# Optimization experiments

Measured on AMD Instinct MI355X. Metric: run time of the kernel, lower is better.

Reference implementation:

```python
import jax, jax.numpy as jnp
import numpy as np

B, S, H, F, E, TOPK = 2, 2048, 1024, 4096, 8, 2


def setup_inputs() -> dict:
    key = jax.random.key(0)
    k0, k1, k2, k3, k4 = jax.random.split(key, 5)
    scale = 0.02
    return {
        "hidden_states": jax.random.normal(k0, (B, S, H), dtype=jnp.float32),
        "gate_w": jax.random.normal(k1, (E, H), dtype=jnp.float32) * scale,
        "w1": jax.random.normal(k2, (E, F, H), dtype=jnp.float32) * scale,
        "w2": jax.random.normal(k3, (E, H, F), dtype=jnp.float32) * scale,
        "w3": jax.random.normal(k4, (E, F, H), dtype=jnp.float32) * scale,
        "top_k": TOPK,
    }


def reference(hidden_states, gate_w, w1, w2, w3, top_k):
    b, s, h = hidden_states.shape
    num_experts = gate_w.shape[0]
    x = hidden_states.reshape(-1, h)                      # [T,H]
    router_logits = x @ gate_w.T                          # [T,E]
    routing = jax.nn.softmax(router_logits.astype(jnp.float32), axis=-1)
    top_w, top_e = jax.lax.top_k(routing, top_k)          # [T,K]
    top_w = top_w / top_w.sum(axis=-1, keepdims=True)     # renormalize over top-k
    top_w = top_w.astype(x.dtype)
    # combine weights [T,E]: zero for unselected experts (faithful to masked dispatch)
    cw = (jax.nn.one_hot(top_e, num_experts, dtype=x.dtype) * top_w[..., None]).sum(axis=1)
    out = jnp.zeros_like(x)
    for e in range(num_experts):  # fixed, small expert count
        inter = jax.nn.silu(x @ w1[e].T) * (x @ w3[e].T)  # [T,F]
        out = out + cw[:, e:e + 1] * (inter @ w2[e].T)
    return out.reshape(b, s, h), router_logits
```

## Files before the change

### kernel.cpp

```cpp
#include <hip/hip_runtime.h>
#include <stdint.h>

#define T 4096
#define HDIM 1024
#define FDIM 4096
#define NE 8
#define MAXROWS 9216

typedef __bf16 bf16x8 __attribute__((ext_vector_type(8)));
typedef float f32x4 __attribute__((ext_vector_type(4)));

__device__ __forceinline__ unsigned short f2bf(float f) {
    unsigned u = __builtin_bit_cast(unsigned, f);
    u += 0x7FFFu + ((u >> 16) & 1u);
    return (unsigned short)(u >> 16);
}

__device__ __forceinline__ void cp16(const void* g, const void* lds) {
    __builtin_amdgcn_global_load_lds(
        (const __attribute__((address_space(1))) unsigned int*)g,
        (__attribute__((address_space(3))) unsigned int*)(unsigned int)(unsigned long long)lds,
        16, 0, 0);
}

__global__ void conv_x_k(const float* __restrict__ x, unsigned short* __restrict__ xb) {
    size_t i = ((size_t)blockIdx.x * 256 + threadIdx.x) * 8;
    float4 a = *(const float4*)(x + i);
    float4 b = *(const float4*)(x + i + 4);
    uint4 v;
    v.x = (unsigned)f2bf(a.x) | ((unsigned)f2bf(a.y) << 16);
    v.y = (unsigned)f2bf(a.z) | ((unsigned)f2bf(a.w) << 16);
    v.z = (unsigned)f2bf(b.x) | ((unsigned)f2bf(b.y) << 16);
    v.w = (unsigned)f2bf(b.z) | ((unsigned)f2bf(b.w) << 16);
    *(uint4*)(xb + i) = v;
}

__global__ void conv_w13_k(const float* __restrict__ src, unsigned short* __restrict__ dst,
                           int f0, int Fc) {
    int e = blockIdx.y;
    size_t rem = ((size_t)blockIdx.x * 256 + threadIdx.x) * 8;
    const float* s = src + ((size_t)e * FDIM + f0) * HDIM + rem;
    unsigned short* d = dst + (size_t)e * Fc * HDIM + rem;
    float4 a = *(const float4*)(s);
    float4 b = *(const float4*)(s + 4);
    uint4 v;
    v.x = (unsigned)f2bf(a.x) | ((unsigned)f2bf(a.y) << 16);
    v.y = (unsigned)f2bf(a.z) | ((unsigned)f2bf(a.w) << 16);
    v.z = (unsigned)f2bf(b.x) | ((unsigned)f2bf(b.y) << 16);
    v.w = (unsigned)f2bf(b.z) | ((unsigned)f2bf(b.w) << 16);
    *(uint4*)(d) = v;
}

__global__ void conv_w2_k(const float* __restrict__ src, unsigned short* __restrict__ dst,
                          int f0, int Fc, int fcShift) {
    int e = blockIdx.y;
    size_t idx = ((size_t)blockIdx.x * 256 + threadIdx.x) * 8;
    int h = (int)(idx >> fcShift);
    int c = (int)(idx & (size_t)(Fc - 1));
    const float* s = src + ((size_t)e * HDIM + h) * FDIM + f0 + c;
    unsigned short* d = dst + (size_t)e * HDIM * Fc + idx;
    float4 a = *(const float4*)(s);
    float4 b = *(const float4*)(s + 4);
    uint4 v;
    v.x = (unsigned)f2bf(a.x) | ((unsigned)f2bf(a.y) << 16);
    v.y = (unsigned)f2bf(a.z) | ((unsigned)f2bf(a.w) << 16);
    v.z = (unsigned)f2bf(b.x) | ((unsigned)f2bf(b.y) << 16);
    v.w = (unsigned)f2bf(b.z) | ((unsigned)f2bf(b.w) << 16);
    *(uint4*)(d) = v;
}

__global__ void router_k(const float* __restrict__ x, const float* __restrict__ gw,
                         float* __restrict__ logits_out, int* __restrict__ cnt,
                         int* __restrict__ list, float* __restrict__ wlist) {
    int w = threadIdx.x >> 6, lane = threadIdx.x & 63;
    int t = blockIdx.x * 4 + w;
    float acc[NE];
#pragma unroll
    for (int e = 0; e < NE; ++e) acc[e] = 0.f;
    for (int i = 0; i < HDIM / 64; ++i) {
        int h = i * 64 + lane;
        float xv = x[(size_t)t * HDIM + h];
#pragma unroll
        for (int e = 0; e < NE; ++e) acc[e] += xv * gw[e * HDIM + h];
    }
#pragma unroll
    for (int e = 0; e < NE; ++e)
#pragma unroll
        for (int off = 32; off; off >>= 1) acc[e] += __shfl_xor(acc[e], off);
    if (lane == 0) {
#pragma unroll
        for (int e = 0; e < NE; ++e) logits_out[(size_t)t * NE + e] = acc[e];
        int e1 = 0;
#pragma unroll
        for (int e = 1; e < NE; ++e) if (acc[e] > acc[e1]) e1 = e;
        int e2 = (e1 == 0) ? 1 : 0;
#pragma unroll
        for (int e = 0; e < NE; ++e) { if (e == e1) continue; if (acc[e] > acc[e2]) e2 = e; }
        float wa = 1.f / (1.f + expf(acc[e2] - acc[e1]));
        float wb = 1.f - wa;
        int p1 = atomicAdd(&cnt[e1], 1); list[e1 * T + p1] = t; wlist[e1 * T + p1] = wa;
        int p2 = atomicAdd(&cnt[e2], 1); list[e2 * T + p2] = t; wlist[e2 * T + p2] = wb;
    }
}

__global__ void offsets_k(const int* __restrict__ cnt, int* __restrict__ poff) {
    if (threadIdx.x == 0) {
        int o = 0; poff[0] = 0;
        for (int e = 0; e < NE; ++e) { o += ((cnt[e] + 127) >> 7) << 7; poff[e + 1] = o; }
    }
}

__global__ void compact_k(const int* __restrict__ cnt, const int* __restrict__ poff,
                          const int* __restrict__ list, const float* __restrict__ wlist,
                          int* __restrict__ tok_row, float* __restrict__ w_row) {
    int gid = blockIdx.x * 256 + threadIdx.x;
    int e = gid >> 12, i = gid & (T - 1);
    int pc = poff[e + 1] - poff[e];
    if (i < pc) {
        int row = poff[e] + i;
        if (i < cnt[e]) { tok_row[row] = list[e * T + i]; w_row[row] = wlist[e * T + i]; }
        else           { tok_row[row] = T;               w_row[row] = 0.f; }
    }
}

__global__ __launch_bounds__(256, 3) void gemm1_k(
    const unsigned short* __restrict__ xb, const unsigned short* __restrict__ wb1,
    const unsigned short* __restrict__ wb3, const int* __restrict__ tok_row,
    const int* __restrict__ poff, unsigned short* __restrict__ inter, int Fc) {

    __shared__ __align__(16) unsigned short As[128 * 64];
    __shared__ __align__(16) unsigned short B1[128 * 64];
    __shared__ __align__(16) unsigned short B3[128 * 64];
    __shared__ int toks[128];
    __shared__ int e_sh;

    int row0 = blockIdx.x * 128;
    if (row0 >= poff[NE]) return;
    int tid = threadIdx.x;
    if (tid == 0) { int e = 0; while (row0 >= poff[e + 1]) ++e; e_sh = e; }
    if (tid < 128) toks[tid] = tok_row[row0 + tid];
    __syncthreads();
    int e = e_sh;
    int fr0 = blockIdx.y * 128;
    const unsigned short* w1p = wb1 + ((size_t)e * Fc + fr0) * HDIM;
    const unsigned short* w3p = wb3 + ((size_t)e * Fc + fr0) * HDIM;

    int wv = tid >> 6, lane = tid & 63;
    int quad = lane >> 4, l16 = lane & 15;
    int wm = (wv >> 1) * 64, wn = (wv & 1) * 64;

    int sr = lane >> 3;
    int sc = (lane & 7) ^ sr;
    unsigned a_off[4];
#pragma unroll
    for (int jj = 0; jj < 4; ++jj)
        a_off[jj] = (unsigned)toks[wv * 32 + jj * 8 + sr] * HDIM + sc * 8;
    const unsigned short* w1b = w1p + (size_t)(wv * 32 + sr) * HDIM + sc * 8;
    const unsigned short* w3b = w3p + (size_t)(wv * 32 + sr) * HDIM + sc * 8;

    f32x4 acc1[4][4], acc3[4][4];
#pragma unroll
    for (int a = 0; a < 4; ++a)
#pragma unroll
        for (int b = 0; b < 4; ++b) {
            acc1[a][b] = f32x4{0.f, 0.f, 0.f, 0.f};
            acc3[a][b] = f32x4{0.f, 0.f, 0.f, 0.f};
        }

    for (int k0 = 0; k0 < HDIM; k0 += 64) {
#pragma unroll
        for (int jj = 0; jj < 4; ++jj) {
            int j = wv * 4 + jj;
            cp16(xb + a_off[jj] + k0, As + j * 512);
            cp16(w1b + (size_t)jj * 8 * HDIM + k0, B1 + j * 512);
            cp16(w3b + (size_t)jj * 8 * HDIM + k0, B3 + j * 512);
        }
        __syncthreads();
#pragma unroll
        for (int ks = 0; ks < 2; ++ks) {
            int cb0 = ks * 4 + quad;
            bf16x8 af[4];
#pragma unroll
            for (int mi = 0; mi < 4; ++mi) {
                int m = wm + mi * 16 + l16;
                af[mi] = *(const bf16x8*)(As + m * 64 + ((cb0 ^ (m & 7)) * 8));
            }
#pragma unroll
            for (int ni = 0; ni < 4; ++ni) {
                int n = wn + ni * 16 + l16;
                int boff = n * 64 + ((cb0 ^ (n & 7)) * 8);
                bf16x8 b1f = *(const bf16x8*)(B1 + boff);
                bf16x8 b3f = *(const bf16x8*)(B3 + boff);
#pragma unroll
                for (int mi = 0; mi < 4; ++mi) {
                    acc1[mi][ni] = __builtin_amdgcn_mfma_f32_16x16x32_bf16(af[mi], b1f, acc1[mi][ni], 0, 0, 0);
                    acc3[mi][ni] = __builtin_amdgcn_mfma_f32_16x16x32_bf16(af[mi], b3f, acc3[mi][ni], 0, 0, 0);
                }
            }
        }
        __syncthreads();
    }
#pragma unroll
    for (int mi = 0; mi < 4; ++mi)
#pragma unroll
        for (int ni = 0; ni < 4; ++ni)
#pragma unroll
            for (int r = 0; r < 4; ++r) {
                int m = wm + mi * 16 + quad * 4 + r;
                int n = wn + ni * 16 + l16;
                float v1 = acc1[mi][ni][r], v3 = acc3[mi][ni][r];
                float hval = (v1 / (1.f + __expf(-v1))) * v3;
                inter[(size_t)(row0 + m) * Fc + fr0 + n] = f2bf(hval);
            }
}

__global__ __launch_bounds__(256, 3) void gemm2_k(
    const unsigned short* __restrict__ inter, const unsigned short* __restrict__ wb2,
    const int* __restrict__ tok_row, const float* __restrict__ w_row,
    const int* __restrict__ poff, float* __restrict__ out, int Fc) {

    __shared__ __align__(16) unsigned short As[128 * 64];
    __shared__ __align__(16) unsigned short Bs[128 * 64];
    __shared__ int e_sh;

    int row0 = blockIdx.x * 128;
    if (row0 >= poff[NE]) return;
    int tid = threadIdx.x;
    if (tid == 0) { int e = 0; while (row0 >= poff[e + 1]) ++e; e_sh = e; }
    __syncthreads();
    int e = e_sh;
    int n0 = blockIdx.y * 128;

    int wv = tid >> 6, lane = tid & 63;
    int quad = lane >> 4, l16 = lane & 15;
    int wm = (wv >> 1) * 64, wn = (wv & 1) * 64;

    int sr = lane >> 3;
    int sc = (lane & 7) ^ sr;
    const unsigned short* a_b = inter + (size_t)(row0 + wv * 32 + sr) * Fc + sc * 8;
    const unsigned short* b_b = wb2 + ((size_t)e * HDIM + n0 + wv * 32 + sr) * Fc + sc * 8;

    f32x4 acc[4][4];
#pragma unroll
    for (int a = 0; a < 4; ++a)
#pragma unroll
        for (int b = 0; b < 4; ++b) acc[a][b] = f32x4{0.f, 0.f, 0.f, 0.f};

    for (int k0 = 0; k0 < Fc; k0 += 64) {
#pragma unroll
        for (int jj = 0; jj < 4; ++jj) {
            int j = wv * 4 + jj;
            cp16(a_b + (size_t)jj * 8 * Fc + k0, As + j * 512);
            cp16(b_b + (size_t)jj * 8 * Fc + k0, Bs + j * 512);
        }
        __syncthreads();
#pragma unroll
        for (int ks = 0; ks < 2; ++ks) {
            int cb0 = ks * 4 + quad;
            bf16x8 af[4];
#pragma unroll
            for (int mi = 0; mi < 4; ++mi) {
                int m = wm + mi * 16 + l16;
                af[mi] = *(const bf16x8*)(As + m * 64 + ((cb0 ^ (m & 7)) * 8));
            }
#pragma unroll
            for (int ni = 0; ni < 4; ++ni) {
                int n = wn + ni * 16 + l16;
                bf16x8 bf = *(const bf16x8*)(Bs + n * 64 + ((cb0 ^ (n & 7)) * 8));
#pragma unroll
                for (int mi = 0; mi < 4; ++mi)
                    acc[mi][ni] = __builtin_amdgcn_mfma_f32_16x16x32_bf16(af[mi], bf, acc[mi][ni], 0, 0, 0);
            }
        }
        __syncthreads();
    }
#pragma unroll
    for (int mi = 0; mi < 4; ++mi)
#pragma unroll
        for (int ni = 0; ni < 4; ++ni)
#pragma unroll
            for (int r = 0; r < 4; ++r) {
                int m = wm + mi * 16 + quad * 4 + r;
                int n = wn + ni * 16 + l16;
                int grow = row0 + m;
                float wr = w_row[grow];
                if (wr != 0.f) {
                    int t = tok_row[grow];
                    atomicAdd(out + (size_t)t * HDIM + n0 + n, wr * acc[mi][ni][r]);
                }
            }
}

extern "C" void kernel_launch(void* const* d_in, const int* in_sizes, int n_in,
                              void* d_out, int out_size, void* d_ws, size_t ws_size,
                              hipStream_t stream) {
    const float* x  = (const float*)d_in[0];
    const float* gw = (const float*)d_in[1];
    const float* w1 = (const float*)d_in[2];
    const float* w2 = (const float*)d_in[3];
    const float* w3 = (const float*)d_in[4];
    float* out = (float*)d_out;
    float* logits = out + (size_t)T * HDIM;

    char* ws = (char*)d_ws;
    size_t off = 0;
    auto alloc = [&](size_t b) {
        off = (off + 255) & ~(size_t)255;
        void* p = ws + off;
        off += b;
        return p;
    };
    int* cnt        = (int*)alloc(NE * 4);
    int* poff       = (int*)alloc((NE + 1) * 4);
    int* list       = (int*)alloc((size_t)NE * T * 4);
    float* wlist    = (float*)alloc((size_t)NE * T * 4);
    int* tok_row    = (int*)alloc(MAXROWS * 4);
    float* w_row    = (float*)alloc(MAXROWS * 4);
    unsigned short* xb = (unsigned short*)alloc((size_t)(T + 1) * HDIM * 2);
    size_t fixed_off = off;

    int Fc = 4096, fcShift = 12;
    for (;;) {
        size_t need = fixed_off + 3 * ((size_t)NE * Fc * HDIM * 2) + (size_t)MAXROWS * Fc * 2 + 1024;
        if (need <= ws_size || Fc == 512) break;
        Fc >>= 1; fcShift -= 1;
    }
    unsigned short* wb1 = (unsigned short*)alloc((size_t)NE * Fc * HDIM * 2);
    unsigned short* wb3 = (unsigned short*)alloc((size_t)NE * Fc * HDIM * 2);
    unsigned short* wb2 = (unsigned short*)alloc((size_t)NE * HDIM * Fc * 2);
    unsigned short* inter = (unsigned short*)alloc((size_t)MAXROWS * Fc * 2);

    hipMemsetAsync(cnt, 0, NE * 4, stream);
    hipMemsetAsync(out, 0, (size_t)T * HDIM * 4, stream);
    hipMemsetAsync(xb + (size_t)T * HDIM, 0, HDIM * 2, stream);
    conv_x_k<<<(T * HDIM / 8) / 256, 256, 0, stream>>>(x, xb);
    router_k<<<T / 4, 256, 0, stream>>>(x, gw, logits, cnt, list, wlist);
    offsets_k<<<1, 64, 0, stream>>>(cnt, poff);
    compact_k<<<NE * T / 256, 256, 0, stream>>>(cnt, poff, list, wlist, tok_row, w_row);

    int nMT = MAXROWS / 128;
    for (int f0 = 0; f0 < FDIM; f0 += Fc) {
        conv_w13_k<<<dim3(Fc / 2, NE), 256, 0, stream>>>(w1, wb1, f0, Fc);
        conv_w13_k<<<dim3(Fc / 2, NE), 256, 0, stream>>>(w3, wb3, f0, Fc);
        conv_w2_k<<<dim3(HDIM * Fc / 2048, NE), 256, 0, stream>>>(w2, wb2, f0, Fc, fcShift);
        gemm1_k<<<dim3(nMT, Fc / 128), 256, 0, stream>>>(xb, wb1, wb3, tok_row, poff, inter, Fc);
        gemm2_k<<<dim3(nMT, HDIM / 128), 256, 0, stream>>>(inter, wb2, tok_row, w_row, poff, out, Fc);
    }
}
```

Before: 847.0 us.

## Widen gemm2 tile to 128x256 with 512 threads and fuse weight conversion

gemm2 now uses 512-thread blocks computing a 128x256 output tile, so each A tile of the intermediate activations is reused across twice as many output columns, halving A reloads. The atomic epilogue is reordered so the row weight and token index are loaded once per row. When the whole F dimension fits in the workspace, the three weight conversions are merged into one launch over all of w1, w3 and w2, and the F-chunk loop is removed. The larger tile adds LDS and register pressure and halves the number of blocks in the y dimension.

```diff
diff --git a/kernel.cpp b/kernel.cpp
--- a/kernel.cpp
+++ b/kernel.cpp
@@ -33,6 +33,24 @@
     v.z = (unsigned)f2bf(b.x) | ((unsigned)f2bf(b.y) << 16);
     v.w = (unsigned)f2bf(b.z) | ((unsigned)f2bf(b.w) << 16);
     *(uint4*)(xb + i) = v;
+}
+
+__global__ void conv_all_k(const float* __restrict__ w1, const float* __restrict__ w3,
+                           const float* __restrict__ w2,
+                           unsigned short* __restrict__ wb1, unsigned short* __restrict__ wb3,
+                           unsigned short* __restrict__ wb2) {
+    int z = blockIdx.y;
+    const float* s = (z == 0) ? w1 : (z == 1) ? w3 : w2;
+    unsigned short* d = (z == 0) ? wb1 : (z == 1) ? wb3 : wb2;
+    size_t i = ((size_t)blockIdx.x * 256 + threadIdx.x) * 8;
+    float4 a = *(const float4*)(s + i);
+    float4 b = *(const float4*)(s + i + 4);
+    uint4 v;
+    v.x = (unsigned)f2bf(a.x) | ((unsigned)f2bf(a.y) << 16);
+    v.y = (unsigned)f2bf(a.z) | ((unsigned)f2bf(a.w) << 16);
+    v.z = (unsigned)f2bf(b.x) | ((unsigned)f2bf(b.y) << 16);
+    v.w = (unsigned)f2bf(b.z) | ((unsigned)f2bf(b.w) << 16);
+    *(uint4*)(d + i) = v;
 }
 
 __global__ void conv_w13_k(const float* __restrict__ src, unsigned short* __restrict__ dst,
@@ -214,13 +232,13 @@
             }
 }
 
-__global__ __launch_bounds__(256, 3) void gemm2_k(
+__global__ __launch_bounds__(512, 4) void gemm2_k(
     const unsigned short* __restrict__ inter, const unsigned short* __restrict__ wb2,
     const int* __restrict__ tok_row, const float* __restrict__ w_row,
     const int* __restrict__ poff, float* __restrict__ out, int Fc) {
 
     __shared__ __align__(16) unsigned short As[128 * 64];
-    __shared__ __align__(16) unsigned short Bs[128 * 64];
+    __shared__ __align__(16) unsigned short Bs[256 * 64];
     __shared__ int e_sh;
 
     int row0 = blockIdx.x * 128;
@@ -229,15 +247,16 @@
     if (tid == 0) { int e = 0; while (row0 >= poff[e + 1]) ++e; e_sh = e; }
     __syncthreads();
     int e = e_sh;
-    int n0 = blockIdx.y * 128;
+    int n0 = blockIdx.y * 256;
 
     int wv = tid >> 6, lane = tid & 63;
     int quad = lane >> 4, l16 = lane & 15;
-    int wm = (wv >> 1) * 64, wn = (wv & 1) * 64;
+    int wm = (wv & 1) * 64;
+    int wn = (wv >> 1) * 64;
 
     int sr = lane >> 3;
     int sc = (lane & 7) ^ sr;
-    const unsigned short* a_b = inter + (size_t)(row0 + wv * 32 + sr) * Fc + sc * 8;
+    const unsigned short* a_b = inter + (size_t)(row0 + wv * 16 + sr) * Fc + sc * 8;
     const unsigned short* b_b = wb2 + ((size_t)e * HDIM + n0 + wv * 32 + sr) * Fc + sc * 8;
 
     f32x4 acc[4][4];
@@ -248,11 +267,11 @@
 
     for (int k0 = 0; k0 < Fc; k0 += 64) {
 #pragma unroll
-        for (int jj = 0; jj < 4; ++jj) {
-            int j = wv * 4 + jj;
-            cp16(a_b + (size_t)jj * 8 * Fc + k0, As + j * 512);
-            cp16(b_b + (size_t)jj * 8 * Fc + k0, Bs + j * 512);
-        }
+        for (int jj = 0; jj < 2; ++jj)
+            cp16(a_b + (size_t)jj * 8 * Fc + k0, As + (wv * 2 + jj) * 512);
+#pragma unroll
+        for (int jj = 0; jj < 4; ++jj)
+            cp16(b_b + (size_t)jj * 8 * Fc + k0, Bs + (wv * 4 + jj) * 512);
         __syncthreads();
 #pragma unroll
         for (int ks = 0; ks < 2; ++ks) {
@@ -277,18 +296,18 @@
 #pragma unroll
     for (int mi = 0; mi < 4; ++mi)
 #pragma unroll
-        for (int ni = 0; ni < 4; ++ni)
-#pragma unroll
-            for (int r = 0; r < 4; ++r) {
-                int m = wm + mi * 16 + quad * 4 + r;
-                int n = wn + ni * 16 + l16;
-                int grow = row0 + m;
-                float wr = w_row[grow];
-                if (wr != 0.f) {
-                    int t = tok_row[grow];
-                    atomicAdd(out + (size_t)t * HDIM + n0 + n, wr * acc[mi][ni][r]);
-                }
-            }
+        for (int r = 0; r < 4; ++r) {
+            int m = wm + mi * 16 + quad * 4 + r;
+            int grow = row0 + m;
+            float wr = w_row[grow];
+            if (wr != 0.f) {
+                int t = tok_row[grow];
+                float* op = out + (size_t)t * HDIM + n0;
+#pragma unroll
+                for (int ni = 0; ni < 4; ++ni)
+                    atomicAdd(op + wn + ni * 16 + l16, wr * acc[mi][ni][r]);
+            }
+        }
 }
 
 extern "C" void kernel_launch(void* const* d_in, const int* in_sizes, int n_in,
@@ -339,11 +358,18 @@
     compact_k<<<NE * T / 256, 256, 0, stream>>>(cnt, poff, list, wlist, tok_row, w_row);
 
     int nMT = MAXROWS / 128;
-    for (int f0 = 0; f0 < FDIM; f0 += Fc) {
-        conv_w13_k<<<dim3(Fc / 2, NE), 256, 0, stream>>>(w1, wb1, f0, Fc);
-        conv_w13_k<<<dim3(Fc / 2, NE), 256, 0, stream>>>(w3, wb3, f0, Fc);
-        conv_w2_k<<<dim3(HDIM * Fc / 2048, NE), 256, 0, stream>>>(w2, wb2, f0, Fc, fcShift);
-        gemm1_k<<<dim3(nMT, Fc / 128), 256, 0, stream>>>(xb, wb1, wb3, tok_row, poff, inter, Fc);
-        gemm2_k<<<dim3(nMT, HDIM / 128), 256, 0, stream>>>(inter, wb2, tok_row, w_row, poff, out, Fc);
-    }
-}
+    if (Fc == FDIM) {
+        conv_all_k<<<dim3((size_t)NE * FDIM * HDIM / 8 / 256, 3), 256, 0, stream>>>(
+            w1, w3, w2, wb1, wb3, wb2);
+        gemm1_k<<<dim3(nMT, FDIM / 128), 256, 0, stream>>>(xb, wb1, wb3, tok_row, poff, inter, FDIM);
+        gemm2_k<<<dim3(nMT, HDIM / 256), 512, 0, stream>>>(inter, wb2, tok_row, w_row, poff, out, FDIM);
+    } else {
+        for (int f0 = 0; f0 < FDIM; f0 += Fc) {
+            conv_w13_k<<<dim3(Fc / 2, NE), 256, 0, stream>>>(w1, wb1, f0, Fc);
+            conv_w13_k<<<dim3(Fc / 2, NE), 256, 0, stream>>>(w3, wb3, f0, Fc);
+            conv_w2_k<<<dim3(HDIM * Fc / 2048, NE), 256, 0, stream>>>(w2, wb2, f0, Fc, fcShift);
+            gemm1_k<<<dim3(nMT, Fc / 128), 256, 0, stream>>>(xb, wb1, wb3, tok_row, poff, inter, Fc);
+            gemm2_k<<<dim3(nMT, HDIM / 256), 512, 0, stream>>>(inter, wb2, tok_row, w_row, poff, out, Fc);
+        }
+    }
+}
```

Measured after the change: 844.2 us. No clear change (-0.3%).
